# Kernel tuning notes

Hardware: AMD Instinct MI355X
Metric: run time of the kernel (lower is better)

## Reference

```python
import jax, jax.numpy as jnp
import numpy as np

D_MODEL = 1024
NUM_HEADS = 16
D_K = D_MODEL // NUM_HEADS


def setup_inputs() -> dict:
    key = jax.random.key(0)
    ks = jax.random.split(key, 9)
    s = 1.0 / np.sqrt(D_MODEL)
    x = jax.random.normal(ks[0], (4, 2048, D_MODEL), dtype=jnp.float32)
    Wq = jax.random.uniform(ks[1], (D_MODEL, D_MODEL), jnp.float32, -s, s)
    bq = jax.random.uniform(ks[2], (D_MODEL,), jnp.float32, -s, s)
    Wk = jax.random.uniform(ks[3], (D_MODEL, D_MODEL), jnp.float32, -s, s)
    bk = jax.random.uniform(ks[4], (D_MODEL,), jnp.float32, -s, s)
    Wv = jax.random.uniform(ks[5], (D_MODEL, D_MODEL), jnp.float32, -s, s)
    bv = jax.random.uniform(ks[6], (D_MODEL,), jnp.float32, -s, s)
    Wo = jax.random.uniform(ks[7], (D_MODEL, D_MODEL), jnp.float32, -s, s)
    bo = jax.random.uniform(ks[8], (D_MODEL,), jnp.float32, -s, s)
    return {"x": x, "Wq": Wq, "bq": bq, "Wk": Wk, "bk": bk,
            "Wv": Wv, "bv": bv, "Wo": Wo, "bo": bo}


def reference(x, Wq, bq, Wk, bk, Wv, bv, Wo, bo):
    B, T, C = x.shape
    H, Dk = NUM_HEADS, D_K
    # linear projections (torch Linear: x @ W.T + b; here W stored as [in,out])
    q = (x @ Wq + bq).reshape(B, T, H, Dk).transpose(0, 2, 1, 3)  # [B,H,T,Dk]
    k = (x @ Wk + bk).reshape(B, T, H, Dk).transpose(0, 2, 1, 3)
    v = (x @ Wv + bv).reshape(B, T, H, Dk).transpose(0, 2, 1, 3)
    scores = jnp.einsum("bhtd,bhsd->bhts", q, k) / jnp.sqrt(jnp.float32(Dk))
    attn = jax.nn.softmax(scores, axis=-1)  # [B,H,T,T]
    context = jnp.einsum("bhts,bhsd->bhtd", attn, v)
    context = context.transpose(0, 2, 1, 3).reshape(B, T, C)
    return context @ Wo + bo
```

## Files before the change

kernel.cpp:

```cpp
#include <hip/hip_runtime.h>
#include <hip/hip_bf16.h>
#include <stdint.h>

typedef short bf16x8 __attribute__((ext_vector_type(8)));
typedef float f32x4  __attribute__((ext_vector_type(4)));

#define MFMA16(a, b, c) __builtin_amdgcn_mfma_f32_16x16x32_bf16((a), (b), (c), 0, 0, 0)

__device__ __forceinline__ unsigned short f2bf(float f) {
    union { float f; unsigned int u; } v; v.f = f;
    unsigned int u = v.u;
    u += 0x7fffu + ((u >> 16) & 1u);
    return (unsigned short)(u >> 16);
}

__device__ __forceinline__ float exp2f_fast(float x) {
#if __has_builtin(__builtin_amdgcn_exp2f)
    return __builtin_amdgcn_exp2f(x);
#else
    return exp2f(x);
#endif
}

__device__ __forceinline__ void g2lds16(const void* g, void* l) {
    __builtin_amdgcn_global_load_lds(
        (const __attribute__((address_space(1))) void*)g,
        (__attribute__((address_space(3))) void*)l, 16, 0, 0);
}


__global__ __launch_bounds__(256) void convert_x_kernel(
    const float4* __restrict__ src, ushort4* __restrict__ dst)
{
    int i = blockIdx.x * 256 + threadIdx.x;
    float4 v = src[i];
    ushort4 o;
    o.x = f2bf(v.x); o.y = f2bf(v.y); o.z = f2bf(v.z); o.w = f2bf(v.w);
    dst[i] = o;
}

__global__ __launch_bounds__(256) void transpose_w_kernel(
    const float* __restrict__ src, unsigned short* __restrict__ dst)
{
    __shared__ float tile[64][65];
    const int k0 = blockIdx.x * 64, n0 = blockIdx.y * 64;
    const int tx = threadIdx.x & 63, ty = threadIdx.x >> 6;
    #pragma unroll
    for (int i = 0; i < 64; i += 4)
        tile[ty + i][tx] = src[(size_t)(k0 + ty + i) * 1024 + n0 + tx];
    __syncthreads();
    #pragma unroll
    for (int i = 0; i < 64; i += 4)
        dst[(size_t)(n0 + ty + i) * 1024 + k0 + tx] = f2bf(tile[tx][ty + i]);
}


#define QSCALE 0.18033688011112042f

template <int MODE>
__global__ __launch_bounds__(256, 2) void gemm_bt(
    const unsigned short* __restrict__ A, const unsigned short* __restrict__ Bt,
    const float* __restrict__ b0, const float* __restrict__ b1, const float* __restrict__ b2,
    unsigned short* __restrict__ Qb, unsigned short* __restrict__ Kb,
    unsigned short* __restrict__ Vt, float* __restrict__ out)
{
    __shared__ alignas(16) unsigned short As[128 * 32];
    __shared__ alignas(16) unsigned short Bs[128 * 32];

    const int t = threadIdx.x;
    const int m0 = blockIdx.y * 128, n0 = blockIdx.x * 128;
    const int lane = t & 63, w = t >> 6, quad = lane >> 4, c16 = lane & 15;
    const int moff = (w >> 1) * 64, noff = (w & 1) * 64;

    f32x4 acc[4][4];
    #pragma unroll
    for (int i = 0; i < 4; ++i)
        #pragma unroll
        for (int j = 0; j < 4; ++j)
            acc[i][j] = (f32x4){0.f, 0.f, 0.f, 0.f};

    const unsigned short* Ag = A + (size_t)(m0 + (t >> 2)) * 1024 + (t & 3) * 8;
    const unsigned short* Bg = Bt + (size_t)(n0 + (t >> 2)) * 1024 + (t & 3) * 8;
    unsigned short* Asl = As + t * 8;
    unsigned short* Bsl = Bs + t * 8;

    for (int k0 = 0; k0 < 1024; k0 += 32) {
        g2lds16(Ag + k0,             Asl);
        g2lds16(Ag + 64 * 1024 + k0, Asl + 2048);
        g2lds16(Bg + k0,             Bsl);
        g2lds16(Bg + 64 * 1024 + k0, Bsl + 2048);
        __syncthreads();

        bf16x8 af[4], bfr[4];
        #pragma unroll
        for (int ms = 0; ms < 4; ++ms)
            af[ms] = *(const bf16x8*)(As + (moff + ms * 16 + c16) * 32 + quad * 8);
        #pragma unroll
        for (int ns = 0; ns < 4; ++ns)
            bfr[ns] = *(const bf16x8*)(Bs + (noff + ns * 16 + c16) * 32 + quad * 8);
        #pragma unroll
        for (int ms = 0; ms < 4; ++ms)
            #pragma unroll
            for (int ns = 0; ns < 4; ++ns)
                acc[ms][ns] = MFMA16(af[ms], bfr[ns], acc[ms][ns]);
        __syncthreads();
    }

    #pragma unroll
    for (int ns = 0; ns < 4; ++ns) {
        const int n = n0 + noff + ns * 16 + c16;
        if (MODE == 0) {
            const int mat = n >> 10, nn = n & 1023;
            const int h = nn >> 6, d = nn & 63;
            const float bias = (mat == 0) ? b0[nn] : ((mat == 1) ? b1[nn] : b2[nn]);
            #pragma unroll
            for (int ms = 0; ms < 4; ++ms) {
                const int mbase = m0 + moff + ms * 16 + quad * 4;
                const int b = mbase >> 11, tbase = mbase & 2047;
                const int bh = b * 16 + h;
                if (mat == 2) {
                    ushort4 pk;
                    pk.x = f2bf(acc[ms][ns][0] + bias);
                    pk.y = f2bf(acc[ms][ns][1] + bias);
                    pk.z = f2bf(acc[ms][ns][2] + bias);
                    pk.w = f2bf(acc[ms][ns][3] + bias);
                    *(ushort4*)(Vt + ((size_t)bh * 64 + d) * 2048 + tbase) = pk;
                } else {
                    #pragma unroll
                    for (int r = 0; r < 4; ++r) {
                        float v = acc[ms][ns][r] + bias;
                        if (mat == 0) v *= QSCALE;
                        unsigned short* dst = (mat == 0) ? Qb : Kb;
                        dst[((size_t)bh * 2048 + tbase + r) * 64 + d] = f2bf(v);
                    }
                }
            }
        } else {
            const float bias = b0[n];
            #pragma unroll
            for (int ms = 0; ms < 4; ++ms) {
                #pragma unroll
                for (int r = 0; r < 4; ++r) {
                    const int m = m0 + moff + ms * 16 + quad * 4 + r;
                    out[(size_t)m * 1024 + n] = acc[ms][ns][r] + bias;
                }
            }
        }
    }
}


__global__ __launch_bounds__(256, 2) void attn_kernel(
    const unsigned short* __restrict__ Qb, const unsigned short* __restrict__ Kb,
    const unsigned short* __restrict__ Vt, unsigned short* __restrict__ ctx)
{
    __shared__ alignas(16) unsigned short Ks[64 * 64];
    __shared__ alignas(16) unsigned short Vs[64 * 64];
    __shared__ alignas(16) unsigned short pl[4][32 * 64];

    const int t = threadIdx.x, w = t >> 6, lane = t & 63;
    const int quad = lane >> 4, c16 = lane & 15;
    const int bh = blockIdx.y, qt = blockIdx.x;
    const int qbase = qt * 128 + w * 32;

    bf16x8 qf[2][2];
    #pragma unroll
    for (int mt = 0; mt < 2; ++mt) {
        const unsigned short* Qp = Qb + ((size_t)bh * 2048 + qbase + mt * 16 + c16) * 64;
        qf[mt][0] = *(const bf16x8*)(Qp + quad * 8);
        qf[mt][1] = *(const bf16x8*)(Qp + 32 + quad * 8);
    }

    float l_r[2][4];
    f32x4 O[2][4];
    #pragma unroll
    for (int mt = 0; mt < 2; ++mt)
        #pragma unroll
        for (int j = 0; j < 4; ++j) { l_r[mt][j] = 0.f; O[mt][j] = (f32x4){0.f, 0.f, 0.f, 0.f}; }

    const int srow = t >> 3;
    const int sgrp = (t & 7) ^ (srow & 7);
    const unsigned short* Kg = Kb + (size_t)bh * 2048 * 64 + (size_t)srow * 64 + sgrp * 8;
    const unsigned short* Vg = Vt + (size_t)bh * 64 * 2048 + (size_t)srow * 2048 + sgrp * 8;
    unsigned short* Ksl = Ks + t * 8;
    unsigned short* Vsl = Vs + t * 8;
    unsigned short* plw = pl[w];
    const f32x4 fzero = {0.f, 0.f, 0.f, 0.f};

    for (int s0 = 0; s0 < 2048; s0 += 64) {
        g2lds16(Kg + s0 * 64,           Ksl);
        g2lds16(Kg + s0 * 64 + 32 * 64, Ksl + 2048);
        g2lds16(Vg + s0,                Vsl);
        g2lds16(Vg + s0 + 32 * 2048,    Vsl + 2048);
        __syncthreads();

        f32x4 sa[2][4];
        #pragma unroll
        for (int ct = 0; ct < 4; ++ct) {
            const int key = ct * 16 + c16;
            const bf16x8 kf0 = *(const bf16x8*)(Ks + key * 64 + ((quad ^ (key & 7)) << 3));
            const bf16x8 kf1 = *(const bf16x8*)(Ks + key * 64 + (((4 + quad) ^ (key & 7)) << 3));
            sa[0][ct] = MFMA16(qf[0][0], kf0, fzero);
            sa[1][ct] = MFMA16(qf[1][0], kf0, fzero);
            sa[0][ct] = MFMA16(qf[0][1], kf1, sa[0][ct]);
            sa[1][ct] = MFMA16(qf[1][1], kf1, sa[1][ct]);
        }

        #pragma unroll
        for (int mt = 0; mt < 2; ++mt)
            #pragma unroll
            for (int ct = 0; ct < 4; ++ct)
                #pragma unroll
                for (int r = 0; r < 4; ++r) {
                    const float p = exp2f_fast(sa[mt][ct][r]);
                    const unsigned short pb = f2bf(p);
                    l_r[mt][r] += __uint_as_float((unsigned int)pb << 16);
                    const int row = mt * 16 + quad * 4 + r;
                    const int grp = ct * 2 + (c16 >> 3);
                    plw[row * 64 + ((grp ^ (row & 7)) << 3) + (c16 & 7)] = pb;
                }
        asm volatile("s_waitcnt lgkmcnt(0)" ::: "memory");

        bf16x8 pa[2][2];
        #pragma unroll
        for (int mt = 0; mt < 2; ++mt) {
            const int row = mt * 16 + c16;
            pa[mt][0] = *(const bf16x8*)(plw + row * 64 + ((quad ^ (row & 7)) << 3));
            pa[mt][1] = *(const bf16x8*)(plw + row * 64 + (((4 + quad) ^ (row & 7)) << 3));
        }
        #pragma unroll
        for (int dc = 0; dc < 4; ++dc) {
            const int d = dc * 16 + c16;
            const bf16x8 vf0 = *(const bf16x8*)(Vs + d * 64 + ((quad ^ (d & 7)) << 3));
            const bf16x8 vf1 = *(const bf16x8*)(Vs + d * 64 + (((4 + quad) ^ (d & 7)) << 3));
            O[0][dc] = MFMA16(pa[0][0], vf0, O[0][dc]);
            O[1][dc] = MFMA16(pa[1][0], vf0, O[1][dc]);
            O[0][dc] = MFMA16(pa[0][1], vf1, O[0][dc]);
            O[1][dc] = MFMA16(pa[1][1], vf1, O[1][dc]);
        }
        __syncthreads();
    }

    #pragma unroll
    for (int off = 1; off < 16; off <<= 1)
        #pragma unroll
        for (int mt = 0; mt < 2; ++mt)
            #pragma unroll
            for (int r = 0; r < 4; ++r)
                l_r[mt][r] += __shfl_xor(l_r[mt][r], off);

    const int b = bh >> 4, h = bh & 15;
    #pragma unroll
    for (int mt = 0; mt < 2; ++mt) {
        float inv[4];
        #pragma unroll
        for (int r = 0; r < 4; ++r) inv[r] = 1.0f / l_r[mt][r];
        #pragma unroll
        for (int dc = 0; dc < 4; ++dc)
            #pragma unroll
            for (int r = 0; r < 4; ++r) {
                const int row = qbase + mt * 16 + quad * 4 + r;
                ctx[((size_t)(b * 2048 + row)) * 1024 + h * 64 + dc * 16 + c16] =
                    f2bf(O[mt][dc][r] * inv[r]);
            }
    }
}


extern "C" void kernel_launch(void* const* d_in, const int* in_sizes, int n_in,
                              void* d_out, int out_size, void* d_ws, size_t ws_size,
                              hipStream_t stream)
{
    const float* x  = (const float*)d_in[0];
    const float* Wq = (const float*)d_in[1];
    const float* bq = (const float*)d_in[2];
    const float* Wk = (const float*)d_in[3];
    const float* bk = (const float*)d_in[4];
    const float* Wv = (const float*)d_in[5];
    const float* bv = (const float*)d_in[6];
    const float* Wo = (const float*)d_in[7];
    const float* bo = (const float*)d_in[8];
    float* out = (float*)d_out;

    char* ws = (char*)d_ws;
    unsigned short* xb    = (unsigned short*)(ws);
    unsigned short* Wqkvt = (unsigned short*)(ws + (16u << 20));
    unsigned short* Wot   = (unsigned short*)(ws + (22u << 20));
    unsigned short* Vt    = (unsigned short*)(ws + (24u << 20));
    unsigned short* Qb    = (unsigned short*)((char*)d_out);
    unsigned short* Kb    = (unsigned short*)((char*)d_out + (16u << 20));

    convert_x_kernel<<<8192, 256, 0, stream>>>((const float4*)x, (ushort4*)xb);
    dim3 tg(16, 16);
    transpose_w_kernel<<<tg, 256, 0, stream>>>(Wq, Wqkvt);
    transpose_w_kernel<<<tg, 256, 0, stream>>>(Wk, Wqkvt + (1u << 20));
    transpose_w_kernel<<<tg, 256, 0, stream>>>(Wv, Wqkvt + (2u << 20));
    transpose_w_kernel<<<tg, 256, 0, stream>>>(Wo, Wot);

    gemm_bt<0><<<dim3(24, 64), 256, 0, stream>>>(xb, Wqkvt, bq, bk, bv, Qb, Kb, Vt, nullptr);
    attn_kernel<<<dim3(16, 64), 256, 0, stream>>>(Qb, Kb, Vt, xb );
    gemm_bt<1><<<dim3(8, 64), 256, 0, stream>>>(xb, Wot, bo, nullptr, nullptr,
                                                nullptr, nullptr, nullptr, out);
}
```

Before: 326.7 us.

## Restructure attention to 2 waves of 64 query rows with transposed score MFMA

The attention kernel now runs 128 threads per block, and each wave handles 64 query rows instead of 32, so every K/V fragment read from LDS feeds twice as many MFMAs. Scores are computed as K·Q^T so each lane holds four consecutive keys for one query row. This lets exp results be packed into bf16 pairs and written with 64-bit LDS stores, and the row sum reduces with only two shuffles. In exchange, register pressure rises (16 O accumulators per wave), there are fewer waves per block to hide load latency, and the row sum now accumulates fp32 probabilities rather than bf16-rounded ones.

```diff
diff --git a/kernel.cpp b/kernel.cpp
--- a/kernel.cpp
+++ b/kernel.cpp
@@ -20,6 +20,10 @@
 #else
     return exp2f(x);
 #endif
+}
+
+__device__ __forceinline__ unsigned int pack_bf2(float a, float b) {
+    return (unsigned int)f2bf(a) | ((unsigned int)f2bf(b) << 16);
 }
 
 __device__ __forceinline__ void g2lds16(const void* g, void* l) {
@@ -150,111 +154,107 @@
 }
 
 
-__global__ __launch_bounds__(256, 2) void attn_kernel(
+__global__ __launch_bounds__(128, 2) void attn_kernel(
     const unsigned short* __restrict__ Qb, const unsigned short* __restrict__ Kb,
     const unsigned short* __restrict__ Vt, unsigned short* __restrict__ ctx)
 {
     __shared__ alignas(16) unsigned short Ks[64 * 64];
     __shared__ alignas(16) unsigned short Vs[64 * 64];
-    __shared__ alignas(16) unsigned short pl[4][32 * 64];
+    __shared__ alignas(16) unsigned short pl[2][64 * 64];
 
     const int t = threadIdx.x, w = t >> 6, lane = t & 63;
     const int quad = lane >> 4, c16 = lane & 15;
-    const int bh = blockIdx.y, qt = blockIdx.x;
-    const int qbase = qt * 128 + w * 32;
-
-    bf16x8 qf[2][2];
-    #pragma unroll
-    for (int mt = 0; mt < 2; ++mt) {
+    const int bh = blockIdx.y;
+    const int qbase = blockIdx.x * 128 + w * 64;
+
+    bf16x8 qf[4][2];
+    #pragma unroll
+    for (int mt = 0; mt < 4; ++mt) {
         const unsigned short* Qp = Qb + ((size_t)bh * 2048 + qbase + mt * 16 + c16) * 64;
         qf[mt][0] = *(const bf16x8*)(Qp + quad * 8);
         qf[mt][1] = *(const bf16x8*)(Qp + 32 + quad * 8);
     }
 
-    float l_r[2][4];
-    f32x4 O[2][4];
-    #pragma unroll
-    for (int mt = 0; mt < 2; ++mt)
-        #pragma unroll
-        for (int j = 0; j < 4; ++j) { l_r[mt][j] = 0.f; O[mt][j] = (f32x4){0.f, 0.f, 0.f, 0.f}; }
-
-    const int srow = t >> 3;
-    const int sgrp = (t & 7) ^ (srow & 7);
-    const unsigned short* Kg = Kb + (size_t)bh * 2048 * 64 + (size_t)srow * 64 + sgrp * 8;
-    const unsigned short* Vg = Vt + (size_t)bh * 64 * 2048 + (size_t)srow * 2048 + sgrp * 8;
+    float l_r[4] = {0.f, 0.f, 0.f, 0.f};
+    f32x4 O[4][4];
+    #pragma unroll
+    for (int mt = 0; mt < 4; ++mt)
+        #pragma unroll
+        for (int dc = 0; dc < 4; ++dc) O[mt][dc] = (f32x4){0.f, 0.f, 0.f, 0.f};
+
+    const int sgrp = (t & 7) ^ ((t >> 3) & 7);
+    const unsigned short* Kgl = Kb + (size_t)bh * 131072 + (size_t)(t >> 3) * 64 + sgrp * 8;
+    const unsigned short* Vgl = Vt + (size_t)bh * 131072 + (size_t)(t >> 3) * 2048 + sgrp * 8;
     unsigned short* Ksl = Ks + t * 8;
     unsigned short* Vsl = Vs + t * 8;
     unsigned short* plw = pl[w];
     const f32x4 fzero = {0.f, 0.f, 0.f, 0.f};
 
     for (int s0 = 0; s0 < 2048; s0 += 64) {
-        g2lds16(Kg + s0 * 64,           Ksl);
-        g2lds16(Kg + s0 * 64 + 32 * 64, Ksl + 2048);
-        g2lds16(Vg + s0,                Vsl);
-        g2lds16(Vg + s0 + 32 * 2048,    Vsl + 2048);
+        #pragma unroll
+        for (int q = 0; q < 4; ++q) {
+            g2lds16(Kgl + s0 * 64 + q * 1024,  Ksl + q * 1024);
+            g2lds16(Vgl + s0 + q * 32768,      Vsl + q * 1024);
+        }
         __syncthreads();
 
-        f32x4 sa[2][4];
         #pragma unroll
         for (int ct = 0; ct < 4; ++ct) {
             const int key = ct * 16 + c16;
             const bf16x8 kf0 = *(const bf16x8*)(Ks + key * 64 + ((quad ^ (key & 7)) << 3));
             const bf16x8 kf1 = *(const bf16x8*)(Ks + key * 64 + (((4 + quad) ^ (key & 7)) << 3));
-            sa[0][ct] = MFMA16(qf[0][0], kf0, fzero);
-            sa[1][ct] = MFMA16(qf[1][0], kf0, fzero);
-            sa[0][ct] = MFMA16(qf[0][1], kf1, sa[0][ct]);
-            sa[1][ct] = MFMA16(qf[1][1], kf1, sa[1][ct]);
+            #pragma unroll
+            for (int mt = 0; mt < 4; ++mt) {
+                f32x4 sa = MFMA16(kf0, qf[mt][0], fzero);
+                sa = MFMA16(kf1, qf[mt][1], sa);
+                const float p0 = exp2f_fast(sa[0]);
+                const float p1 = exp2f_fast(sa[1]);
+                const float p2 = exp2f_fast(sa[2]);
+                const float p3 = exp2f_fast(sa[3]);
+                l_r[mt] += (p0 + p1) + (p2 + p3);
+                uint2 pk;
+                pk.x = pack_bf2(p0, p1);
+                pk.y = pack_bf2(p2, p3);
+                const int row = mt * 16 + c16;
+                const int grp = ct * 2 + (quad >> 1);
+                *(uint2*)(plw + row * 64 + ((grp ^ (row & 7)) << 3) + (quad & 1) * 4) = pk;
+            }
         }
-
-        #pragma unroll
-        for (int mt = 0; mt < 2; ++mt)
-            #pragma unroll
-            for (int ct = 0; ct < 4; ++ct)
+        asm volatile("s_waitcnt lgkmcnt(0)" ::: "memory");
+
+        #pragma unroll
+        for (int kt = 0; kt < 2; ++kt) {
+            bf16x8 pa[4];
+            #pragma unroll
+            for (int mt = 0; mt < 4; ++mt) {
+                const int row = mt * 16 + c16;
+                pa[mt] = *(const bf16x8*)(plw + row * 64 + (((kt * 4 + quad) ^ (row & 7)) << 3));
+            }
+            #pragma unroll
+            for (int dc = 0; dc < 4; ++dc) {
+                const int d = dc * 16 + c16;
+                const bf16x8 vf = *(const bf16x8*)(Vs + d * 64 + (((kt * 4 + quad) ^ (d & 7)) << 3));
                 #pragma unroll
-                for (int r = 0; r < 4; ++r) {
-                    const float p = exp2f_fast(sa[mt][ct][r]);
-                    const unsigned short pb = f2bf(p);
-                    l_r[mt][r] += __uint_as_float((unsigned int)pb << 16);
-                    const int row = mt * 16 + quad * 4 + r;
-                    const int grp = ct * 2 + (c16 >> 3);
-                    plw[row * 64 + ((grp ^ (row & 7)) << 3) + (c16 & 7)] = pb;
-                }
-        asm volatile("s_waitcnt lgkmcnt(0)" ::: "memory");
-
-        bf16x8 pa[2][2];
-        #pragma unroll
-        for (int mt = 0; mt < 2; ++mt) {
-            const int row = mt * 16 + c16;
-            pa[mt][0] = *(const bf16x8*)(plw + row * 64 + ((quad ^ (row & 7)) << 3));
-            pa[mt][1] = *(const bf16x8*)(plw + row * 64 + (((4 + quad) ^ (row & 7)) << 3));
-        }
-        #pragma unroll
-        for (int dc = 0; dc < 4; ++dc) {
-            const int d = dc * 16 + c16;
-            const bf16x8 vf0 = *(const bf16x8*)(Vs + d * 64 + ((quad ^ (d & 7)) << 3));
-            const bf16x8 vf1 = *(const bf16x8*)(Vs + d * 64 + (((4 + quad) ^ (d & 7)) << 3));
-            O[0][dc] = MFMA16(pa[0][0], vf0, O[0][dc]);
-            O[1][dc] = MFMA16(pa[1][0], vf0, O[1][dc]);
-            O[0][dc] = MFMA16(pa[0][1], vf1, O[0][dc]);
-            O[1][dc] = MFMA16(pa[1][1], vf1, O[1][dc]);
+                for (int mt = 0; mt < 4; ++mt)
+                    O[mt][dc] = MFMA16(pa[mt], vf, O[mt][dc]);
+            }
         }
         __syncthreads();
     }
 
     #pragma unroll
-    for (int off = 1; off < 16; off <<= 1)
-        #pragma unroll
-        for (int mt = 0; mt < 2; ++mt)
-            #pragma unroll
-            for (int r = 0; r < 4; ++r)
-                l_r[mt][r] += __shfl_xor(l_r[mt][r], off);
+    for (int mt = 0; mt < 4; ++mt) {
+        l_r[mt] += __shfl_xor(l_r[mt], 16);
+        l_r[mt] += __shfl_xor(l_r[mt], 32);
+    }
 
     const int b = bh >> 4, h = bh & 15;
     #pragma unroll
-    for (int mt = 0; mt < 2; ++mt) {
+    for (int mt = 0; mt < 4; ++mt) {
         float inv[4];
         #pragma unroll
-        for (int r = 0; r < 4; ++r) inv[r] = 1.0f / l_r[mt][r];
+        for (int r = 0; r < 4; ++r)
+            inv[r] = 1.0f / __shfl(l_r[mt], quad * 4 + r);
         #pragma unroll
         for (int dc = 0; dc < 4; ++dc)
             #pragma unroll
@@ -298,7 +298,7 @@
     transpose_w_kernel<<<tg, 256, 0, stream>>>(Wo, Wot);
 
     gemm_bt<0><<<dim3(24, 64), 256, 0, stream>>>(xb, Wqkvt, bq, bk, bv, Qb, Kb, Vt, nullptr);
-    attn_kernel<<<dim3(16, 64), 256, 0, stream>>>(Qb, Kb, Vt, xb );
+    attn_kernel<<<dim3(16, 64), 128, 0, stream>>>(Qb, Kb, Vt, xb );
     gemm_bt<1><<<dim3(8, 64), 256, 0, stream>>>(xb, Wot, bo, nullptr, nullptr,
                                                 nullptr, nullptr, nullptr, out);
 }
```

New measurement: 308.6 us. 1.06x faster.
